# Optimization experiments

Measured on AMD Instinct MI355X. Metric: run time of the kernel, lower is better.

## Reference

```python
import jax, jax.numpy as jnp
import numpy as np

BIN_SZ = 0.02

def setup_inputs() -> dict:
    T, B, D, L, C, H, S = 128, 256, 128, 32, 64, 256, 16
    key = jax.random.key(0)
    ks = iter(jax.random.split(key, 64))
    def nrm(shape, fan_in):
        return jax.random.normal(next(ks), shape, dtype=jnp.float32) / np.float32(np.sqrt(fan_in))
    return dict(
        xs_pre=jax.random.randint(next(ks), (B, T, D), 0, 5).astype(jnp.float32),
        eps0=jax.random.normal(next(ks), (S, B, L), dtype=jnp.float32),
        dW=jax.random.normal(next(ks), (T - 1, S, B, L), dtype=jnp.float32),
        gru_Wih=nrm((3 * H, D), D), gru_Whh=nrm((3 * H, H), H),
        gru_bih=jnp.zeros(3 * H), gru_bhh=jnp.zeros(3 * H),
        enc_W=nrm((C, H), H), enc_b=jnp.zeros(C),
        qz0_W=nrm((2 * L, C), C), qz0_b=jnp.zeros(2 * L),
        fW1=nrm((H, L + C), L + C), fb1=jnp.zeros(H),
        fW2=nrm((H, H), H), fb2=jnp.zeros(H),
        fW3=nrm((L, H), H), fb3=jnp.zeros(L),
        hW1=nrm((H, L), L), hb1=jnp.zeros(H),
        hW2=nrm((H, H), H), hb2=jnp.zeros(H),
        hW3=nrm((L, H), H), hb3=jnp.zeros(L),
        gW1=nrm((L, H), 1), gb1=jnp.zeros((L, H)),
        gW2=nrm((L, H), H), gb2=jnp.zeros(L),
        pz0_mean=jnp.zeros((1, L)), pz0_logstd=jnp.zeros((1, L)),
        C_out=nrm((L, D), L), d_out=jnp.zeros(D),
    )

def _forward(xs_pre, eps0, dW, gru_Wih, gru_Whh, gru_bih, gru_bhh, enc_W, enc_b,
             qz0_W, qz0_b, fW1, fb1, fW2, fb2, fW3, fb3, hW1, hb1, hW2, hb2, hW3, hb3,
             gW1, gb1, gW2, gb2, pz0_mean, pz0_logstd, C_out, d_out):
    xs = jnp.transpose(xs_pre, (1, 0, 2))  # (T,B,D) time-major
    T, B, D = xs.shape
    # --- Encoder: GRU over time-reversed data, linear head, flip back ---
    def gru_step(h, x):
        gi = x @ gru_Wih.T + gru_bih
        gh = h @ gru_Whh.T + gru_bhh
        i_r, i_z, i_n = jnp.split(gi, 3, axis=-1)
        h_r, h_z, h_n = jnp.split(gh, 3, axis=-1)
        r = jax.nn.sigmoid(i_r + h_r)
        u = jax.nn.sigmoid(i_z + h_z)
        n = jnp.tanh(i_n + r * h_n)
        hn = (1.0 - u) * n + u * h
        return hn, hn
    h0 = jnp.zeros((B, gru_Whh.shape[1]), xs.dtype)
    _, hs = jax.lax.scan(gru_step, h0, xs[::-1])
    ctx = (hs @ enc_W.T + enc_b)[::-1]  # (T,B,C)
    # --- initial latent z0 ~ q(z0) ---
    q = ctx[0] @ qz0_W.T + qz0_b
    qz0_mean, qz0_logstd = jnp.split(q, 2, axis=-1)
    z0 = qz0_mean + jnp.exp(qz0_logstd) * eps0  # (S,B,L)
    sp = jax.nn.softplus
    def f_net(i): return sp(sp(i @ fW1.T + fb1) @ fW2.T + fb2) @ fW3.T + fb3
    def h_net(y): return sp(sp(y @ hW1.T + hb1) @ hW2.T + hb2) @ hW3.T + hb3
    def g_fn(y):
        hg = sp(y[..., None] * gW1 + gb1)  # (...,L,H): all diagonal g_nets batched
        return jax.nn.sigmoid(jnp.einsum('...lh,lh->...l', hg, gW2) + gb2) + 0.01
    dt = BIN_SZ
    sq_dt = jnp.sqrt(jnp.asarray(dt, z0.dtype))
    # torchsde euler + searchsorted(right=True): step k uses ctx[min(k+1, T-1)]
    ctx_steps = ctx[jnp.minimum(jnp.arange(T - 1) + 1, T - 1)]  # (T-1,B,C)
    S = z0.shape[0]
    def euler_step(z, inp):
        ctx_i, dw = inp
        ctx_b = jnp.broadcast_to(ctx_i[None], (S,) + ctx_i.shape)
        fv = f_net(jnp.concatenate([z, ctx_b], axis=-1))
        hv = h_net(z)
        gv = g_fn(z)
        u = (fv - hv) / gv
        dlog = 0.5 * jnp.sum(u * u, axis=-1) * dt  # (S,B) logqp increment
        zn = z + fv * dt + gv * (sq_dt * dw)
        return zn, (zn, dlog)
    _, (z_tail, log_ratio) = jax.lax.scan(euler_step, z0, (ctx_steps, dW))
    zs = jnp.concatenate([z0[None], z_tail], axis=0)  # (T,S,B,L)
    zs = jnp.transpose(zs, (1, 0, 2, 3))              # (S,T,B,L)
    log_ratio = jnp.transpose(log_ratio, (1, 0, 2))   # (S,T-1,B)
    # --- Poisson likelihood, rate = bin_sz * exp(linear readout) ---
    log_rate = zs @ C_out + d_out + jnp.log(jnp.asarray(dt, zs.dtype))  # (S,T,B,D)
    ell = xs * log_rate - jnp.exp(log_rate) - jax.lax.lgamma(xs + 1.0)
    log_pxs = ell.sum(-1).sum(1).mean()
    # --- KL(q(z0) || p(z0)) for diagonal Gaussians ---
    kl0 = (pz0_logstd - qz0_logstd
           + (jnp.exp(2.0 * qz0_logstd) + (qz0_mean - pz0_mean) ** 2) / (2.0 * jnp.exp(2.0 * pz0_logstd))
           - 0.5)
    logqp0 = kl0.sum(-1).mean()
    logqp_path = log_ratio.sum(1).mean()
    loss = -log_pxs + logqp0 + logqp_path
    zs_t = jnp.transpose(zs, (0, 2, 1, 3))  # (S,B,T,L)
    m = zs_t.mean(0)
    P_diag = jnp.var(zs_t, axis=0, ddof=1)  # torch.var is unbiased
    return loss, zs_t, m, P_diag

def reference(xs_pre, eps0, dW, gru_Wih, gru_Whh, gru_bih, gru_bhh, enc_W, enc_b,
              qz0_W, qz0_b, fW1, fb1, fW2, fb2, fW3, fb3, hW1, hb1, hW2, hb2, hW3, hb3,
              gW1, gb1, gW2, gb2, pz0_mean, pz0_logstd, C_out, d_out):
    return _forward(xs_pre, eps0, dW, gru_Wih, gru_Whh, gru_bih, gru_bhh, enc_W, enc_b,
                    qz0_W, qz0_b, fW1, fb1, fW2, fb2, fW3, fb3, hW1, hb1, hW2, hb2, hW3, hb3,
                    gW1, gb1, gW2, gb2, pz0_mean, pz0_logstd, C_out, d_out)
```

## Files before the change

### kernel.cpp

```cpp
#include <hip/hip_runtime.h>
#include <math.h>

#define T_ 128
#define B_ 256
#define D_ 128
#define L_ 32
#define C_ 64
#define H_ 256
#define S_ 16
#define R_ 4096
#define NT_ 127
#define DT 0.02f
#define SQDT 0.14142135623730951f

typedef _Float16 h2 __attribute__((ext_vector_type(2)));
typedef _Float16 f16x8 __attribute__((ext_vector_type(8)));
typedef float f32x4m __attribute__((ext_vector_type(4)));
union UH { unsigned u; h2 h; };
union HS { _Float16 f; unsigned short s; };
union U4F { uint4 u; f16x8 h; };

__device__ __forceinline__ float d2(unsigned a, unsigned b, float c){
  UH ua; ua.u = a; UH ub; ub.u = b;
#if defined(__has_builtin)
#if __has_builtin(__builtin_amdgcn_fdot2)
  return __builtin_amdgcn_fdot2(ua.h, ub.h, c, false);
#else
  return fmaf((float)ua.h.x, (float)ub.h.x, fmaf((float)ua.h.y, (float)ub.h.y, c));
#endif
#else
  return fmaf((float)ua.h.x, (float)ub.h.x, fmaf((float)ua.h.y, (float)ub.h.y, c));
#endif
}
__device__ __forceinline__ unsigned pk2(float x, float y){
  UH u; u.h = (h2){(_Float16)x, (_Float16)y}; return u.u;
}
__device__ __forceinline__ unsigned short h1(float x){
  HS t; t.f = (_Float16)x; return t.s;
}
__device__ __forceinline__ float h2f(unsigned short s){
  HS t; t.s = s; return (float)t.f;
}
__device__ __forceinline__ f32x4m mfma16(f16x8 a, f16x8 b, f32x4m c){
  return __builtin_amdgcn_mfma_f32_16x16x32_f16(a, b, c, 0, 0, 0);
}
__device__ __forceinline__ f16x8 ldfragL(const unsigned short* p){
  U4F t; t.u = *(const uint4*)p; return t.h;
}
__device__ __forceinline__ f16x8 ldfragG(const uint4* p){
  U4F t; t.u = *p; return t.h;
}
__device__ __forceinline__ f16x8 ldfragR(uint4 v){
  U4F t; t.u = v; return t.h;
}

__device__ __forceinline__ float sp_(float x){
  return fmaxf(x, 0.f) + __logf(1.f + __expf(-fabsf(x)));
}
__device__ __forceinline__ float sig_(float x){
  return 1.f / (1.f + __expf(-x));
}
__device__ __forceinline__ void dacc4(unsigned av, uint4 w, float a[4]){
  a[0]=d2(av,w.x,a[0]); a[1]=d2(av,w.y,a[1]); a[2]=d2(av,w.z,a[2]); a[3]=d2(av,w.w,a[3]);
}

__device__ __forceinline__ void blk_reduce_add(float v, double* acc){
  for (int o = 32; o > 0; o >>= 1) v += __shfl_down(v, o, 64);
  __shared__ float wpart[4];
  int lane = threadIdx.x & 63, w = threadIdx.x >> 6;
  if (lane == 0) wpart[w] = v;
  __syncthreads();
  if (threadIdx.x == 0) atomicAdd(acc, (double)(wpart[0] + wpart[1] + wpart[2] + wpart[3]));
}

__device__ void do_prep(int i,
                        const float* __restrict__ Wih, const float* __restrict__ Whh,
                        const float* __restrict__ encW,
                        const float* __restrict__ fW1, const float* __restrict__ hW1,
                        const float* __restrict__ fW2, const float* __restrict__ hW2,
                        const float* __restrict__ fW3, const float* __restrict__ hW3,
                        unsigned* WihH, unsigned* WhhH, float* encWT,
                        uint4* fW1B, uint4* hW1B, uint4* fW2B, uint4* hW2B,
                        uint4* fW3B, uint4* hW3B){
  if (i < 49152){ int dp = i / 768, j = i % 768;
    WihH[i] = pk2(Wih[j*128 + 2*dp], Wih[j*128 + 2*dp + 1]); return; }
  i -= 49152;
  if (i < 98304){ int kp = i / 768, j = i % 768;
    WhhH[i] = pk2(Whh[j*256 + 2*kp], Whh[j*256 + 2*kp + 1]); return; }
  i -= 98304;
  if (i < 16384){ int k2 = i >> 6, c = i & 63; encWT[i] = encW[c*256 + k2]; return; }
  i -= 16384;
  if (i < 3072){
    int jt = i / 192, r = i % 192, s = r >> 6, lane = r & 63;
    int col = jt*16 + (lane & 15), kb = s*32 + (lane >> 4)*8;
    const float* src = fW1 + col*96 + kb;
    uint4 v; v.x = pk2(src[0],src[1]); v.y = pk2(src[2],src[3]);
    v.z = pk2(src[4],src[5]); v.w = pk2(src[6],src[7]);
    fW1B[i] = v; return; }
  i -= 3072;
  if (i < 1024){
    int jt = i >> 6, lane = i & 63;
    int col = jt*16 + (lane & 15), kb = (lane >> 4)*8;
    const float* src = hW1 + col*32 + kb;
    uint4 v; v.x = pk2(src[0],src[1]); v.y = pk2(src[2],src[3]);
    v.z = pk2(src[4],src[5]); v.w = pk2(src[6],src[7]);
    hW1B[i] = v; return; }
  i -= 1024;
  if (i < 8192){
    int jt = i >> 9, r = i & 511, s = r >> 6, lane = r & 63;
    int col = jt*16 + (lane & 15), kb = s*32 + (lane >> 4)*8;
    const float* src = fW2 + col*256 + kb;
    uint4 v; v.x = pk2(src[0],src[1]); v.y = pk2(src[2],src[3]);
    v.z = pk2(src[4],src[5]); v.w = pk2(src[6],src[7]);
    fW2B[i] = v; return; }
  i -= 8192;
  if (i < 8192){
    int jt = i >> 9, r = i & 511, s = r >> 6, lane = r & 63;
    int col = jt*16 + (lane & 15), kb = s*32 + (lane >> 4)*8;
    const float* src = hW2 + col*256 + kb;
    uint4 v; v.x = pk2(src[0],src[1]); v.y = pk2(src[2],src[3]);
    v.z = pk2(src[4],src[5]); v.w = pk2(src[6],src[7]);
    hW2B[i] = v; return; }
  i -= 8192;
  if (i < 1024){
    int jt = i >> 9, r = i & 511, s = r >> 6, lane = r & 63;
    int col = jt*16 + (lane & 15), kb = s*32 + (lane >> 4)*8;
    const float* src = fW3 + col*256 + kb;
    uint4 v; v.x = pk2(src[0],src[1]); v.y = pk2(src[2],src[3]);
    v.z = pk2(src[4],src[5]); v.w = pk2(src[6],src[7]);
    fW3B[i] = v; return; }
  i -= 1024;
  if (i < 1024){
    int jt = i >> 9, r = i & 511, s = r >> 6, lane = r & 63;
    int col = jt*16 + (lane & 15), kb = s*32 + (lane >> 4)*8;
    const float* src = hW3 + col*256 + kb;
    uint4 v; v.x = pk2(src[0],src[1]); v.y = pk2(src[2],src[3]);
    v.z = pk2(src[4],src[5]); v.w = pk2(src[6],src[7]);
    hW3B[i] = v; return; }
}

__global__ __launch_bounds__(256) void k_pre(
    const float* __restrict__ Wih, const float* __restrict__ Whh,
    const float* __restrict__ encW,
    const float* __restrict__ fW1, const float* __restrict__ hW1,
    const float* __restrict__ fW2, const float* __restrict__ hW2,
    const float* __restrict__ fW3, const float* __restrict__ hW3,
    const float* __restrict__ gW1, const float* __restrict__ gb1,
    const float* __restrict__ gW2, const float* __restrict__ gb2,
    unsigned* WihH, unsigned* WhhH, float* encWT,
    uint4* fW1B, uint4* hW1B, uint4* fW2B, uint4* hW2B,
    uint4* fW3B, uint4* hW3B, float* gtab, double* accs){
  if (blockIdx.x == 727 && threadIdx.x < 3) accs[threadIdx.x] = 0.0;
  do_prep(blockIdx.x * 256 + threadIdx.x,
          Wih, Whh, encW, fW1, hW1, fW2, hW2, fW3, hW3,
          WihH, WhhH, encWT, fW1B, hW1B, fW2B, hW2B, fW3B, hW3B);
  if (blockIdx.x < 256){
    int l = blockIdx.x >> 3;
    int e = (blockIdx.x & 7) * 256 + threadIdx.x;
    float z = -16.f + (float)e * (1.f / 64.f);
    const float* w1 = gW1 + l * 256;
    const float* b1 = gb1 + l * 256;
    const float* w2 = gW2 + l * 256;
    float s = 0.f;
    #pragma unroll 4
    for (int h = 0; h < 256; ++h)
      s = fmaf(sp_(fmaf(z, w1[h], b1[h])), w2[h], s);
    gtab[l * 2048 + e] = sig_(s + gb2[l]) + 0.01f;
  }
}

__global__ __launch_bounds__(256) void k_gix(
    const float* __restrict__ xs_pre, const unsigned* __restrict__ WihH,
    unsigned short* __restrict__ gixH){
  int kk = blockIdx.x >> 4;
  int b0 = (blockIdx.x & 15) * 16;
  int tid = threadIdx.x;
  int t = 127 - kk;
  __shared__ unsigned x_s[16][64];
  for (int i = tid; i < 16*64; i += 256){
    int r = i >> 6, dp = i & 63;
    const float* xp = xs_pre + ((size_t)(b0 + r)*128 + t)*128 + dp*2;
    x_s[r][dp] = pk2(xp[0], xp[1]);
  }
  __syncthreads();
  float a0[16], a1[16], a2[16];
  #pragma unroll
  for (int r = 0; r < 16; ++r){ a0[r]=0.f; a1[r]=0.f; a2[r]=0.f; }
  for (int dp = 0; dp < 64; ++dp){
    unsigned w0 = WihH[dp*768 + tid];
    unsigned w1 = WihH[dp*768 + 256 + tid];
    unsigned w2 = WihH[dp*768 + 512 + tid];
    #pragma unroll
    for (int r = 0; r < 16; ++r){
      unsigned xv = x_s[r][dp];
      a0[r] = d2(xv, w0, a0[r]);
      a1[r] = d2(xv, w1, a1[r]);
      a2[r] = d2(xv, w2, a2[r]);
    }
  }
  #pragma unroll
  for (int r = 0; r < 16; ++r){
    size_t base = ((size_t)kk*256 + b0 + r)*768;
    gixH[base + tid]       = h1(a0[r]);
    gixH[base + 256 + tid] = h1(a1[r]);
    gixH[base + 512 + tid] = h1(a2[r]);
  }
}

__global__ __launch_bounds__(512, 1) void k_gru_rec(
    const unsigned* __restrict__ WhhH, const float* __restrict__ bih,
    const float* __restrict__ bhh, const unsigned short* __restrict__ gixH,
    float* __restrict__ hsT){
  int tid = threadIdx.x;
  int ks = tid >> 6;
  int lane = tid & 63;
  int j4 = lane * 4;
  int b = blockIdx.x;

  __shared__ float h_s[256];
  __shared__ unsigned h_sH[128];
  __shared__ __align__(16) float part[3][8][256];

  if (tid < 256) h_s[tid] = 0.f;
  if (tid < 128) h_sH[tid] = 0u;

  uint4 w0[16], w1[16], w2[16];
  #pragma unroll
  for (int i = 0; i < 16; ++i){
    const unsigned* wr = WhhH + (ks*16 + i)*768;
    w0[i] = *(const uint4*)(wr + j4);
    w1[i] = *(const uint4*)(wr + 256 + j4);
    w2[i] = *(const uint4*)(wr + 512 + j4);
  }
  __syncthreads();

  for (int k = 0; k < T_; ++k){
    unsigned short pr = 0, pz = 0, pn = 0;
    if (tid < 256){
      size_t gb = ((size_t)k*256 + b)*768;
      pr = gixH[gb + tid];
      pz = gixH[gb + 256 + tid];
      pn = gixH[gb + 512 + tid];
    }
    float a0[4]={0,0,0,0}, a1[4]={0,0,0,0}, a3[4]={0,0,0,0};
    #pragma unroll
    for (int i = 0; i < 16; ++i){
      unsigned hv = h_sH[ks*16 + i];
      dacc4(hv, w0[i], a0);
      dacc4(hv, w1[i], a1);
      dacc4(hv, w2[i], a3);
    }
    *(float4*)&part[0][ks][j4] = make_float4(a0[0],a0[1],a0[2],a0[3]);
    *(float4*)&part[1][ks][j4] = make_float4(a1[0],a1[1],a1[2],a1[3]);
    *(float4*)&part[2][ks][j4] = make_float4(a3[0],a3[1],a3[2],a3[3]);
    __syncthreads();
    if (tid < 256){
      int jj = tid;
      float s0=0.f, s1=0.f, s3=0.f;
      #pragma unroll
      for (int q = 0; q < 8; ++q){
        s0 += part[0][q][jj]; s1 += part[1][q][jj]; s3 += part[2][q][jj];
      }
      float gr = s0 + h2f(pr) + bih[jj] + bhh[jj];
      float gz = s1 + h2f(pz) + bih[256 + jj] + bhh[256 + jj];
      float gnx = h2f(pn) + bih[512 + jj];
      float gnh = s3 + bhh[512 + jj];
      float rr = sig_(gr);
      float uu = sig_(gz);
      float nn = 1.f - 2.f / (1.f + __expf(2.f * (gnx + rr * gnh)));
      float hn = (1.f - uu) * nn + uu * h_s[jj];
      hsT[((size_t)k*256 + b)*256 + jj] = hn;
      h_s[jj] = hn;
      float hnb = __shfl_down(hn, 1, 64);
      if ((tid & 1) == 0) h_sH[jj >> 1] = pk2(hn, hnb);
    }
    __syncthreads();
  }
}

__global__ __launch_bounds__(256) void k_ctx2(
    const float* __restrict__ hsT, const float* __restrict__ encWT,
    const float* __restrict__ encb, float* __restrict__ ctx2){
  int t = blockIdx.x >> 4;
  int b0 = (blockIdx.x & 15) * 16;
  int tid = threadIdx.x;
  __shared__ float h_s[16][256];
  int kk0 = 127 - t;
  for (int i = tid; i < 4096; i += 256){
    int rr = i >> 8, jj = i & 255;
    h_s[rr][jj] = hsT[((size_t)kk0*256 + b0 + rr)*256 + jj];
  }
  __syncthreads();
  float acc0=0, acc1=0, acc2=0, acc3=0;
  int c = tid & 63;
  int bq0 = tid >> 6;
  #pragma unroll 4
  for (int kk = 0; kk < 256; ++kk){
    float wv = encWT[kk*64 + c];
    acc0 = fmaf(h_s[bq0][kk],      wv, acc0);
    acc1 = fmaf(h_s[bq0 + 4][kk],  wv, acc1);
    acc2 = fmaf(h_s[bq0 + 8][kk],  wv, acc2);
    acc3 = fmaf(h_s[bq0 + 12][kk], wv, acc3);
  }
  float bv = encb[c];
  ctx2[(t*256 + b0 + bq0)*64 + c]      = acc0 + bv;
  ctx2[(t*256 + b0 + bq0 + 4)*64 + c]  = acc1 + bv;
  ctx2[(t*256 + b0 + bq0 + 8)*64 + c]  = acc2 + bv;
  ctx2[(t*256 + b0 + bq0 + 12)*64 + c] = acc3 + bv;
}

__global__ __launch_bounds__(256) void k_q0z0(
    const float* __restrict__ ctx2, const float* __restrict__ qW,
    const float* __restrict__ qb, const float* __restrict__ pm,
    const float* __restrict__ pls, const float* __restrict__ eps0,
    float* __restrict__ zs, double* __restrict__ kl_acc){
  int b0 = blockIdx.x * 16;
  int tid = threadIdx.x;
  int lb = tid >> 4;
  int lp = tid & 15;
  int b = b0 + lb;
  __shared__ float qm_s[16][32], qls_s[16][32];
  const float* crow = ctx2 + b * 64;
  float am0 = qb[lp],      as0 = qb[32 + lp];
  float am1 = qb[16 + lp], as1 = qb[48 + lp];
  const float* wm0 = qW + lp * 64;
  const float* ws0 = qW + (32 + lp) * 64;
  const float* wm1 = qW + (16 + lp) * 64;
  const float* ws1 = qW + (48 + lp) * 64;
  for (int c = 0; c < 64; ++c){
    float cv = crow[c];
    am0 = fmaf(cv, wm0[c], am0); as0 = fmaf(cv, ws0[c], as0);
    am1 = fmaf(cv, wm1[c], am1); as1 = fmaf(cv, ws1[c], as1);
  }
  qm_s[lb][lp] = am0;      qls_s[lb][lp] = as0;
  qm_s[lb][16 + lp] = am1; qls_s[lb][16 + lp] = as1;
  float kl = 0.f;
  {
    float plsl = pls[lp], pml = pm[lp];
    float dm = am0 - pml;
    kl += plsl - as0 + (__expf(2.f*as0) + dm*dm) / (2.f*__expf(2.f*plsl)) - 0.5f;
    plsl = pls[16 + lp]; pml = pm[16 + lp];
    dm = am1 - pml;
    kl += plsl - as1 + (__expf(2.f*as1) + dm*dm) / (2.f*__expf(2.f*plsl)) - 0.5f;
  }
  blk_reduce_add(kl, kl_acc);
  int s = tid >> 4, bb = tid & 15;
  int r = s * 256 + b0 + bb;
  #pragma unroll
  for (int l = 0; l < 32; l += 4){
    float4 e = *(const float4*)(eps0 + (size_t)r*32 + l);
    float4 z;
    z.x = fmaf(__expf(qls_s[bb][l    ]), e.x, qm_s[bb][l    ]);
    z.y = fmaf(__expf(qls_s[bb][l + 1]), e.y, qm_s[bb][l + 1]);
    z.z = fmaf(__expf(qls_s[bb][l + 2]), e.z, qm_s[bb][l + 2]);
    z.w = fmaf(__expf(qls_s[bb][l + 3]), e.w, qm_s[bb][l + 3]);
    *(float4*)(zs + (size_t)r * (T_ * L_) + l) = z;
  }
}

__global__ __launch_bounds__(512, 1) void k_sde_all(
    const float* __restrict__ ctx2,
    const uint4* __restrict__ fW1B, const float* __restrict__ fb1,
    const uint4* __restrict__ hW1B, const float* __restrict__ hb1,
    const uint4* __restrict__ fW2B, const float* __restrict__ fb2,
    const uint4* __restrict__ hW2B, const float* __restrict__ hb2,
    const uint4* __restrict__ fW3B, const uint4* __restrict__ hW3B,
    const float* __restrict__ fb3, const float* __restrict__ hb3,
    const float* __restrict__ gtab,
    const float* __restrict__ dW, float* __restrict__ zs,
    double* __restrict__ u2_acc){
  int tid = threadIdx.x;
  int r0 = blockIdx.x * 16;
  int b0 = r0 & 255;
  int w  = tid >> 6;
  int ln = tid & 63;
  int frow = ln & 15;
  int kg = ln >> 4;
  int crow0 = kg * 4;
  int lane32 = tid & 31;
  int row16 = tid >> 5;

  __shared__ __align__(16) unsigned short z_sH[16][32];
  __shared__ __align__(16) unsigned short ctx_sH[16][64];
  __shared__ __align__(16) unsigned short a1H[2][16][256];
  __shared__ __align__(16) unsigned short a2H[2][16][256];
  __shared__ float fh_part[2][2][16][32];

  float zreg = zs[(size_t)(r0 + row16) * 4096 + lane32];
  {
    int idx = row16*32 + (((((lane32) >> 3) ^ (row16 & 3)) << 3) | (lane32 & 7));
    ((unsigned short*)z_sH)[idx] = h1(zreg);
  }
  float u2loc = 0.f;

  uint4 wf2r[16], wh2r[16];
  #pragma unroll
  for (int q = 0; q < 2; ++q){
    #pragma unroll
    for (int s = 0; s < 8; ++s){
      wf2r[q*8 + s] = fW2B[((2*w + q)*8 + s)*64 + ln];
      wh2r[q*8 + s] = hW2B[((2*w + q)*8 + s)*64 + ln];
    }
  }

  const unsigned short* a1b0 = &a1H[0][0][0];
  const unsigned short* a1b1 = &a1H[1][0][0];
  const unsigned short* a2b0 = &a2H[0][0][0];
  const unsigned short* a2b1 = &a2H[1][0][0];

  for (int k = 0; k < NT_; ++k){
    __syncthreads();
    if (tid < 256){
      int rr = tid >> 4, c4 = (tid & 15) * 4;
      float4 v = *(const float4*)(ctx2 + ((size_t)(k + 1)*256 + b0 + rr)*64 + c4);
      uint2 p = make_uint2(pk2(v.x, v.y), pk2(v.z, v.w));
      int idx = rr*64 + ((((c4 >> 3) ^ (rr & 7)) << 3) | (c4 & 7));
      *(uint2*)(((unsigned short*)ctx_sH) + idx) = p;
    }
    __syncthreads();

    float gv;
    {
      float tpos = fminf(fmaxf((zreg + 16.f) * 64.f, 0.f), 2046.99f);
      int i0 = (int)tpos;
      float fr = tpos - (float)i0;
      const float* tl = gtab + lane32 * 2048 + i0;
      float t0 = tl[0], t1 = tl[1];
      gv = fmaf(fr, t1 - t0, t0);
    }

    {
      f16x8 zA  = ldfragL(((const unsigned short*)z_sH) + frow*32 + ((kg ^ (frow & 3)) << 3));
      f16x8 cA0 = ldfragL(((const unsigned short*)ctx_sH) + frow*64 + (((kg       ) ^ (frow & 7)) << 3));
      f16x8 cA1 = ldfragL(((const unsigned short*)ctx_sH) + frow*64 + (((4 + kg   ) ^ (frow & 7)) << 3));
      #pragma unroll
      for (int q = 0; q < 2; ++q){
        int jt = 2*w + q;
        const uint4* bp = fW1B + (jt*3)*64 + ln;
        f32x4m acc = {0.f, 0.f, 0.f, 0.f};
        acc = mfma16(zA,  ldfragG(bp),        acc);
        acc = mfma16(cA0, ldfragG(bp + 64),   acc);
        acc = mfma16(cA1, ldfragG(bp + 128),  acc);
        int col = jt*16 + frow;
        float bv = fb1[col];
        #pragma unroll
        for (int r = 0; r < 4; ++r){
          int row = crow0 + r;
          ((unsigned short*)a1H)[0*4096 + row*256 + ((((col >> 3) ^ (row & 7)) << 3) | (col & 7))]
            = h1(sp_(acc[r] + bv));
        }
      }
      #pragma unroll
      for (int q = 0; q < 2; ++q){
        int jt = 2*w + q;
        f32x4m acc = {0.f, 0.f, 0.f, 0.f};
        acc = mfma16(zA, ldfragG(hW1B + jt*64 + ln), acc);
        int col = jt*16 + frow;
        float bv = hb1[col];
        #pragma unroll
        for (int r = 0; r < 4; ++r){
          int row = crow0 + r;
          ((unsigned short*)a1H)[1*4096 + row*256 + ((((col >> 3) ^ (row & 7)) << 3) | (col & 7))]
            = h1(sp_(acc[r] + bv));
        }
      }
    }
    __syncthreads();

    {
      f16x8 fr8[8];
      #pragma unroll
      for (int s = 0; s < 8; ++s)
        fr8[s] = ldfragL(a1b0 + frow*256 + (((s*4 + kg) ^ (frow & 7)) << 3));
      #pragma unroll
      for (int q = 0; q < 2; ++q){
        int jt = 2*w + q;
        f32x4m acc = {0.f, 0.f, 0.f, 0.f};
        #pragma unroll
        for (int s = 0; s < 8; ++s)
          acc = mfma16(fr8[s], ldfragR(wf2r[q*8 + s]), acc);
        int col = jt*16 + frow;
        float bv = fb2[col];
        #pragma unroll
        for (int r = 0; r < 4; ++r){
          int row = crow0 + r;
          ((unsigned short*)a2H)[0*4096 + row*256 + ((((col >> 3) ^ (row & 7)) << 3) | (col & 7))]
            = h1(sp_(acc[r] + bv));
        }
      }
      #pragma unroll
      for (int s = 0; s < 8; ++s)
        fr8[s] = ldfragL(a1b1 + frow*256 + (((s*4 + kg) ^ (frow & 7)) << 3));
      #pragma unroll
      for (int q = 0; q < 2; ++q){
        int jt = 2*w + q;
        f32x4m acc = {0.f, 0.f, 0.f, 0.f};
        #pragma unroll
        for (int s = 0; s < 8; ++s)
          acc = mfma16(fr8[s], ldfragR(wh2r[q*8 + s]), acc);
        int col = jt*16 + frow;
        float bv = hb2[col];
        #pragma unroll
        for (int r = 0; r < 4; ++r){
          int row = crow0 + r;
          ((unsigned short*)a2H)[1*4096 + row*256 + ((((col >> 3) ^ (row & 7)) << 3) | (col & 7))]
            = h1(sp_(acc[r] + bv));
        }
      }
    }
    __syncthreads();

    {
      int kh  = w >> 2;
      int net = (w >> 1) & 1;
      int jt  = w & 1;
      const unsigned short* ab = net ? a2b1 : a2b0;
      const uint4* bb = (net ? hW3B : fW3B) + (jt*8 + kh*4)*64 + ln;
      f32x4m acc = {0.f, 0.f, 0.f, 0.f};
      #pragma unroll
      for (int q = 0; q < 4; ++q){
        int s = kh*4 + q;
        f16x8 af = ldfragL(ab + frow*256 + (((s*4 + kg) ^ (frow & 7)) << 3));
        acc = mfma16(af, ldfragG(bb + q*64), acc);
      }
      int col = jt*16 + frow;
      #pragma unroll
      for (int r = 0; r < 4; ++r)
        fh_part[kh][net][crow0 + r][col] = acc[r];
    }
    __syncthreads();

    {
      float fv = fh_part[0][0][row16][lane32] + fh_part[1][0][row16][lane32] + fb3[lane32];
      float hv = fh_part[0][1][row16][lane32] + fh_part[1][1][row16][lane32] + hb3[lane32];
      float uu = (fv - hv) / gv;
      u2loc = fmaf(uu, uu, u2loc);
      int rr = r0 + row16;
      float dwv = dW[((size_t)k*4096 + rr)*32 + lane32];
      float zn = zreg + fv*DT + gv*(SQDT*dwv);
      zreg = zn;
      zs[((size_t)rr*128 + (k + 1))*32 + lane32] = zn;
      int idx = row16*32 + ((((lane32 >> 3) ^ (row16 & 3)) << 3) | (lane32 & 7));
      ((unsigned short*)z_sH)[idx] = h1(zn);
    }
  }

  for (int o = 32; o > 0; o >>= 1) u2loc += __shfl_down(u2loc, o, 64);
  __shared__ float wp[8];
  if ((tid & 63) == 0) wp[tid >> 6] = u2loc;
  __syncthreads();
  if (tid == 0){
    float s = 0.f;
    #pragma unroll
    for (int q = 0; q < 8; ++q) s += wp[q];
    atomicAdd(u2_acc, (double)s);
  }
}

__global__ __launch_bounds__(256) void k_poismv(
    const float* __restrict__ zs, const float* __restrict__ Cw,
    const float* __restrict__ db, const float* __restrict__ xs_pre,
    double* __restrict__ ell_acc, float* __restrict__ m, float* __restrict__ P){
  if (blockIdx.x < 4096){
    const int N = S_ * B_ * T_ * D_;
    const int stride = 4096 * 256;
    float local = 0.f;
    for (int i = blockIdx.x * 256 + threadIdx.x; i < N; i += stride){
      int d = i & 127; int row = i >> 7;
      int t = row & 127; int b = (row >> 7) & 255;
      const float* zrow = zs + (size_t)row * L_;
      float lr = db[d] - 3.912023005428146f;
      #pragma unroll 8
      for (int l = 0; l < L_; ++l) lr = fmaf(zrow[l], Cw[l * D_ + d], lr);
      float xv = xs_pre[(b * T_ + t) * D_ + d];
      int xi = (int)(xv + 0.5f);
      float lg = (xi <= 1) ? 0.f : (xi == 2 ? 0.6931471805599453f :
                 (xi == 3 ? 1.791759469228055f : 3.1780538303479458f));
      local += xv * lr - __expf(lr) - lg;
    }
    blk_reduce_add(local, ell_acc);
  } else {
    int i = (blockIdx.x - 4096) * 256 + threadIdx.x;
    float x[S_];
    float s = 0.f;
    #pragma unroll
    for (int q = 0; q < S_; ++q){ x[q] = zs[(size_t)q * (B_ * T_ * L_) + i]; s += x[q]; }
    float mu = s * (1.f / S_);
    float v = 0.f;
    #pragma unroll
    for (int q = 0; q < S_; ++q){ float dd = x[q] - mu; v = fmaf(dd, dd, v); }
    m[i] = mu;
    P[i] = v * (1.f / (S_ - 1));
  }
}

__global__ void k_fin(const double* __restrict__ accs, float* __restrict__ out){
  double log_pxs = accs[0] / 4096.0;
  double logqp0 = accs[1] / 256.0;
  double logqp_path = 0.5 * 0.02 * accs[2] / 4096.0;
  out[0] = (float)(-log_pxs + logqp0 + logqp_path);
}

extern "C" void kernel_launch(void* const* d_in, const int* in_sizes, int n_in,
                              void* d_out, int out_size, void* d_ws, size_t ws_size,
                              hipStream_t stream) {
  const float* xs_pre = (const float*)d_in[0];
  const float* eps0   = (const float*)d_in[1];
  const float* dW     = (const float*)d_in[2];
  const float* Wih    = (const float*)d_in[3];
  const float* Whh    = (const float*)d_in[4];
  const float* bih    = (const float*)d_in[5];
  const float* bhh    = (const float*)d_in[6];
  const float* encW   = (const float*)d_in[7];
  const float* encb   = (const float*)d_in[8];
  const float* qW     = (const float*)d_in[9];
  const float* qb     = (const float*)d_in[10];
  const float* fW1    = (const float*)d_in[11];
  const float* fb1    = (const float*)d_in[12];
  const float* fW2    = (const float*)d_in[13];
  const float* fb2    = (const float*)d_in[14];
  const float* fW3    = (const float*)d_in[15];
  const float* fb3    = (const float*)d_in[16];
  const float* hW1    = (const float*)d_in[17];
  const float* hb1    = (const float*)d_in[18];
  const float* hW2    = (const float*)d_in[19];
  const float* hb2    = (const float*)d_in[20];
  const float* hW3    = (const float*)d_in[21];
  const float* hb3    = (const float*)d_in[22];
  const float* gW1    = (const float*)d_in[23];
  const float* gb1    = (const float*)d_in[24];
  const float* gW2    = (const float*)d_in[25];
  const float* gb2    = (const float*)d_in[26];
  const float* pm     = (const float*)d_in[27];
  const float* pls    = (const float*)d_in[28];
  const float* Cw     = (const float*)d_in[29];
  const float* db     = (const float*)d_in[30];

  float* out = (float*)d_out;
  float* zs  = out + 1;
  float* m   = out + 1 + 16777216;
  float* P   = m + 1048576;

  unsigned short* gixH = (unsigned short*)zs;

  double* accs = (double*)d_ws;
  float* wf = (float*)d_ws + 16;
  float* hsT   = wf; wf += T_ * B_ * H_;
  float* ctx2  = wf; wf += T_ * B_ * C_;
  unsigned* WihH = (unsigned*)wf; wf += 49152;
  unsigned* WhhH = (unsigned*)wf; wf += 98304;
  float* encWT = wf; wf += 16384;
  uint4* fW1B = (uint4*)wf; wf += 12288;
  uint4* hW1B = (uint4*)wf; wf += 4096;
  uint4* fW2B = (uint4*)wf; wf += 32768;
  uint4* hW2B = (uint4*)wf; wf += 32768;
  uint4* fW3B = (uint4*)wf; wf += 4096;
  uint4* hW3B = (uint4*)wf; wf += 4096;
  float* gtab  = wf; wf += 65536;
  size_t need = (size_t)(wf - (float*)d_ws) * 4;
  if (ws_size < need) return;

  k_pre<<<728, 256, 0, stream>>>(Wih, Whh, encW, fW1, hW1, fW2, hW2, fW3, hW3,
                                 gW1, gb1, gW2, gb2,
                                 WihH, WhhH, encWT, fW1B, hW1B, fW2B, hW2B,
                                 fW3B, hW3B, gtab, accs);
  k_gix<<<2048, 256, 0, stream>>>(xs_pre, WihH, gixH);
  k_gru_rec<<<256, 512, 0, stream>>>(WhhH, bih, bhh, gixH, hsT);
  k_ctx2<<<2048, 256, 0, stream>>>(hsT, encWT, encb, ctx2);
  k_q0z0<<<16, 256, 0, stream>>>(ctx2, qW, qb, pm, pls, eps0, zs, accs + 1);
  k_sde_all<<<256, 512, 0, stream>>>(ctx2,
                                     fW1B, fb1, hW1B, hb1,
                                     fW2B, fb2, hW2B, hb2,
                                     fW3B, hW3B, fb3, hb3,
                                     gtab, dW, zs, accs + 2);
  k_poismv<<<8192, 256, 0, stream>>>(zs, Cw, db, xs_pre, accs + 0, m, P);
  k_fin<<<1, 1, 0, stream>>>(accs, out);
}
```

Before: 1.279 ms.

## Fuse GRU input projection into recurrence and merge small tail kernels

The GRU input-projection kernel is folded into the recurrent kernel: each block now computes its own batch row's input gates from an LDS-staged copy of the time-reversed inputs before running the recurrence. The q(z0)/z0 sampling work moves into the t==0 blocks of the context projection kernel, and the final loss reduction moves into the Poisson/moments kernel through an atomic ticket held in a fourth accumulator slot. This removes three kernel launches and the ctx2 re-read for z0. In exchange, the input projection runs on only 256 single-occupancy blocks with an uneven split, since only half the threads handle the third gate, instead of 2048 well-occupied blocks. The gate results also still round-trip through global memory.

Result: slower. 2.035 ms (+59.1%).

```diff
diff --git a/kernel.cpp b/kernel.cpp
--- a/kernel.cpp
+++ b/kernel.cpp
@@ -150,7 +150,7 @@
     unsigned* WihH, unsigned* WhhH, float* encWT,
     uint4* fW1B, uint4* hW1B, uint4* fW2B, uint4* hW2B,
     uint4* fW3B, uint4* hW3B, float* gtab, double* accs){
-  if (blockIdx.x == 727 && threadIdx.x < 3) accs[threadIdx.x] = 0.0;
+  if (blockIdx.x == 727 && threadIdx.x < 4) accs[threadIdx.x] = 0.0;
   do_prep(blockIdx.x * 256 + threadIdx.x,
           Wih, Whh, encW, fW1, hW1, fW2, hW2, fW3, hW3,
           WihH, WhhH, encWT, fW1B, hW1B, fW2B, hW2B, fW3B, hW3B);
@@ -169,61 +169,66 @@
   }
 }
 
-__global__ __launch_bounds__(256) void k_gix(
+__global__ __launch_bounds__(512, 1) void k_gru_all2(
     const float* __restrict__ xs_pre, const unsigned* __restrict__ WihH,
-    unsigned short* __restrict__ gixH){
-  int kk = blockIdx.x >> 4;
-  int b0 = (blockIdx.x & 15) * 16;
-  int tid = threadIdx.x;
-  int t = 127 - kk;
-  __shared__ unsigned x_s[16][64];
-  for (int i = tid; i < 16*64; i += 256){
-    int r = i >> 6, dp = i & 63;
-    const float* xp = xs_pre + ((size_t)(b0 + r)*128 + t)*128 + dp*2;
-    x_s[r][dp] = pk2(xp[0], xp[1]);
-  }
-  __syncthreads();
-  float a0[16], a1[16], a2[16];
-  #pragma unroll
-  for (int r = 0; r < 16; ++r){ a0[r]=0.f; a1[r]=0.f; a2[r]=0.f; }
-  for (int dp = 0; dp < 64; ++dp){
-    unsigned w0 = WihH[dp*768 + tid];
-    unsigned w1 = WihH[dp*768 + 256 + tid];
-    unsigned w2 = WihH[dp*768 + 512 + tid];
-    #pragma unroll
-    for (int r = 0; r < 16; ++r){
-      unsigned xv = x_s[r][dp];
-      a0[r] = d2(xv, w0, a0[r]);
-      a1[r] = d2(xv, w1, a1[r]);
-      a2[r] = d2(xv, w2, a2[r]);
-    }
-  }
-  #pragma unroll
-  for (int r = 0; r < 16; ++r){
-    size_t base = ((size_t)kk*256 + b0 + r)*768;
-    gixH[base + tid]       = h1(a0[r]);
-    gixH[base + 256 + tid] = h1(a1[r]);
-    gixH[base + 512 + tid] = h1(a2[r]);
-  }
-}
-
-__global__ __launch_bounds__(512, 1) void k_gru_rec(
     const unsigned* __restrict__ WhhH, const float* __restrict__ bih,
-    const float* __restrict__ bhh, const unsigned short* __restrict__ gixH,
+    const float* __restrict__ bhh, unsigned short* __restrict__ gixH,
     float* __restrict__ hsT){
   int tid = threadIdx.x;
+  int b = blockIdx.x;
+
+  __shared__ unsigned x_all[128][64];
+  __shared__ float h_s[256];
+  __shared__ unsigned h_sH[128];
+  __shared__ __align__(16) float part[3][8][256];
+
+  for (int i = tid; i < 8192; i += 512){
+    int t = i >> 6, dp = i & 63;
+    const float* xp = xs_pre + ((size_t)b*128 + t)*128 + dp*2;
+    x_all[127 - t][dp] = pk2(xp[0], xp[1]);
+  }
+  if (tid < 256) h_s[tid] = 0.f;
+  if (tid < 128) h_sH[tid] = 0u;
+  __syncthreads();
+
+  {
+    int j = tid;
+    for (int kc = 0; kc < 128; kc += 16){
+      float acc[16];
+      #pragma unroll
+      for (int q = 0; q < 16; ++q) acc[q] = 0.f;
+      for (int dp = 0; dp < 64; ++dp){
+        unsigned w = WihH[dp*768 + j];
+        #pragma unroll
+        for (int q = 0; q < 16; ++q)
+          acc[q] = d2(x_all[kc + q][dp], w, acc[q]);
+      }
+      #pragma unroll
+      for (int q = 0; q < 16; ++q)
+        gixH[((size_t)(kc + q)*256 + b)*768 + j] = h1(acc[q]);
+    }
+  }
+  if (tid < 256){
+    int j = 512 + tid;
+    for (int kc = 0; kc < 128; kc += 16){
+      float acc[16];
+      #pragma unroll
+      for (int q = 0; q < 16; ++q) acc[q] = 0.f;
+      for (int dp = 0; dp < 64; ++dp){
+        unsigned w = WihH[dp*768 + j];
+        #pragma unroll
+        for (int q = 0; q < 16; ++q)
+          acc[q] = d2(x_all[kc + q][dp], w, acc[q]);
+      }
+      #pragma unroll
+      for (int q = 0; q < 16; ++q)
+        gixH[((size_t)(kc + q)*256 + b)*768 + j] = h1(acc[q]);
+    }
+  }
+
   int ks = tid >> 6;
   int lane = tid & 63;
   int j4 = lane * 4;
-  int b = blockIdx.x;
-
-  __shared__ float h_s[256];
-  __shared__ unsigned h_sH[128];
-  __shared__ __align__(16) float part[3][8][256];
-
-  if (tid < 256) h_s[tid] = 0.f;
-  if (tid < 128) h_sH[tid] = 0u;
-
   uint4 w0[16], w1[16], w2[16];
   #pragma unroll
   for (int i = 0; i < 16; ++i){
@@ -278,9 +283,13 @@
   }
 }
 
-__global__ __launch_bounds__(256) void k_ctx2(
+__global__ __launch_bounds__(256) void k_ctx2q(
     const float* __restrict__ hsT, const float* __restrict__ encWT,
-    const float* __restrict__ encb, float* __restrict__ ctx2){
+    const float* __restrict__ encb, float* __restrict__ ctx2,
+    const float* __restrict__ qW, const float* __restrict__ qb,
+    const float* __restrict__ pm, const float* __restrict__ pls,
+    const float* __restrict__ eps0, float* __restrict__ zs,
+    double* __restrict__ kl_acc){
   int t = blockIdx.x >> 4;
   int b0 = (blockIdx.x & 15) * 16;
   int tid = threadIdx.x;
@@ -303,58 +312,58 @@
     acc3 = fmaf(h_s[bq0 + 12][kk], wv, acc3);
   }
   float bv = encb[c];
-  ctx2[(t*256 + b0 + bq0)*64 + c]      = acc0 + bv;
-  ctx2[(t*256 + b0 + bq0 + 4)*64 + c]  = acc1 + bv;
-  ctx2[(t*256 + b0 + bq0 + 8)*64 + c]  = acc2 + bv;
-  ctx2[(t*256 + b0 + bq0 + 12)*64 + c] = acc3 + bv;
-}
-
-__global__ __launch_bounds__(256) void k_q0z0(
-    const float* __restrict__ ctx2, const float* __restrict__ qW,
-    const float* __restrict__ qb, const float* __restrict__ pm,
-    const float* __restrict__ pls, const float* __restrict__ eps0,
-    float* __restrict__ zs, double* __restrict__ kl_acc){
-  int b0 = blockIdx.x * 16;
-  int tid = threadIdx.x;
-  int lb = tid >> 4;
-  int lp = tid & 15;
-  int b = b0 + lb;
-  __shared__ float qm_s[16][32], qls_s[16][32];
-  const float* crow = ctx2 + b * 64;
-  float am0 = qb[lp],      as0 = qb[32 + lp];
-  float am1 = qb[16 + lp], as1 = qb[48 + lp];
-  const float* wm0 = qW + lp * 64;
-  const float* ws0 = qW + (32 + lp) * 64;
-  const float* wm1 = qW + (16 + lp) * 64;
-  const float* ws1 = qW + (48 + lp) * 64;
-  for (int c = 0; c < 64; ++c){
-    float cv = crow[c];
-    am0 = fmaf(cv, wm0[c], am0); as0 = fmaf(cv, ws0[c], as0);
-    am1 = fmaf(cv, wm1[c], am1); as1 = fmaf(cv, ws1[c], as1);
-  }
-  qm_s[lb][lp] = am0;      qls_s[lb][lp] = as0;
-  qm_s[lb][16 + lp] = am1; qls_s[lb][16 + lp] = as1;
-  float kl = 0.f;
-  {
-    float plsl = pls[lp], pml = pm[lp];
-    float dm = am0 - pml;
-    kl += plsl - as0 + (__expf(2.f*as0) + dm*dm) / (2.f*__expf(2.f*plsl)) - 0.5f;
-    plsl = pls[16 + lp]; pml = pm[16 + lp];
-    dm = am1 - pml;
-    kl += plsl - as1 + (__expf(2.f*as1) + dm*dm) / (2.f*__expf(2.f*plsl)) - 0.5f;
-  }
-  blk_reduce_add(kl, kl_acc);
-  int s = tid >> 4, bb = tid & 15;
-  int r = s * 256 + b0 + bb;
-  #pragma unroll
-  for (int l = 0; l < 32; l += 4){
-    float4 e = *(const float4*)(eps0 + (size_t)r*32 + l);
-    float4 z;
-    z.x = fmaf(__expf(qls_s[bb][l    ]), e.x, qm_s[bb][l    ]);
-    z.y = fmaf(__expf(qls_s[bb][l + 1]), e.y, qm_s[bb][l + 1]);
-    z.z = fmaf(__expf(qls_s[bb][l + 2]), e.z, qm_s[bb][l + 2]);
-    z.w = fmaf(__expf(qls_s[bb][l + 3]), e.w, qm_s[bb][l + 3]);
-    *(float4*)(zs + (size_t)r * (T_ * L_) + l) = z;
+  acc0 += bv; acc1 += bv; acc2 += bv; acc3 += bv;
+  ctx2[(t*256 + b0 + bq0)*64 + c]      = acc0;
+  ctx2[(t*256 + b0 + bq0 + 4)*64 + c]  = acc1;
+  ctx2[(t*256 + b0 + bq0 + 8)*64 + c]  = acc2;
+  ctx2[(t*256 + b0 + bq0 + 12)*64 + c] = acc3;
+
+  if (t == 0){
+    __shared__ float ctx_l[16][64];
+    __shared__ float qm_s[16][32], qls_s[16][32];
+    ctx_l[bq0][c]      = acc0;
+    ctx_l[bq0 + 4][c]  = acc1;
+    ctx_l[bq0 + 8][c]  = acc2;
+    ctx_l[bq0 + 12][c] = acc3;
+    __syncthreads();
+    int lb = tid >> 4;
+    int lp = tid & 15;
+    const float* crow = ctx_l[lb];
+    float am0 = qb[lp],      as0 = qb[32 + lp];
+    float am1 = qb[16 + lp], as1 = qb[48 + lp];
+    const float* wm0 = qW + lp * 64;
+    const float* ws0 = qW + (32 + lp) * 64;
+    const float* wm1 = qW + (16 + lp) * 64;
+    const float* ws1 = qW + (48 + lp) * 64;
+    for (int cc = 0; cc < 64; ++cc){
+      float cv = crow[cc];
+      am0 = fmaf(cv, wm0[cc], am0); as0 = fmaf(cv, ws0[cc], as0);
+      am1 = fmaf(cv, wm1[cc], am1); as1 = fmaf(cv, ws1[cc], as1);
+    }
+    qm_s[lb][lp] = am0;      qls_s[lb][lp] = as0;
+    qm_s[lb][16 + lp] = am1; qls_s[lb][16 + lp] = as1;
+    float kl = 0.f;
+    {
+      float plsl = pls[lp], pml = pm[lp];
+      float dm = am0 - pml;
+      kl += plsl - as0 + (__expf(2.f*as0) + dm*dm) / (2.f*__expf(2.f*plsl)) - 0.5f;
+      plsl = pls[16 + lp]; pml = pm[16 + lp];
+      dm = am1 - pml;
+      kl += plsl - as1 + (__expf(2.f*as1) + dm*dm) / (2.f*__expf(2.f*plsl)) - 0.5f;
+    }
+    blk_reduce_add(kl, kl_acc);
+    int s = tid >> 4, bb = tid & 15;
+    int r = s * 256 + b0 + bb;
+    #pragma unroll
+    for (int l = 0; l < 32; l += 4){
+      float4 e = *(const float4*)(eps0 + (size_t)r*32 + l);
+      float4 z;
+      z.x = fmaf(__expf(qls_s[bb][l    ]), e.x, qm_s[bb][l    ]);
+      z.y = fmaf(__expf(qls_s[bb][l + 1]), e.y, qm_s[bb][l + 1]);
+      z.z = fmaf(__expf(qls_s[bb][l + 2]), e.z, qm_s[bb][l + 2]);
+      z.w = fmaf(__expf(qls_s[bb][l + 3]), e.w, qm_s[bb][l + 3]);
+      *(float4*)(zs + (size_t)r * (T_ * L_) + l) = z;
+    }
   }
 }
 
@@ -560,7 +569,8 @@
 __global__ __launch_bounds__(256) void k_poismv(
     const float* __restrict__ zs, const float* __restrict__ Cw,
     const float* __restrict__ db, const float* __restrict__ xs_pre,
-    double* __restrict__ ell_acc, float* __restrict__ m, float* __restrict__ P){
+    double* __restrict__ accs, float* __restrict__ m, float* __restrict__ P,
+    float* __restrict__ out){
   if (blockIdx.x < 4096){
     const int N = S_ * B_ * T_ * D_;
     const int stride = 4096 * 256;
@@ -578,7 +588,7 @@
                  (xi == 3 ? 1.791759469228055f : 3.1780538303479458f));
       local += xv * lr - __expf(lr) - lg;
     }
-    blk_reduce_add(local, ell_acc);
+    blk_reduce_add(local, accs + 0);
   } else {
     int i = (blockIdx.x - 4096) * 256 + threadIdx.x;
     float x[S_];
@@ -592,13 +602,17 @@
     m[i] = mu;
     P[i] = v * (1.f / (S_ - 1));
   }
-}
-
-__global__ void k_fin(const double* __restrict__ accs, float* __restrict__ out){
-  double log_pxs = accs[0] / 4096.0;
-  double logqp0 = accs[1] / 256.0;
-  double logqp_path = 0.5 * 0.02 * accs[2] / 4096.0;
-  out[0] = (float)(-log_pxs + logqp0 + logqp_path);
+  __threadfence();
+  if (threadIdx.x == 0){
+    unsigned* ticket = (unsigned*)(accs + 3);
+    unsigned tk = atomicAdd(ticket, 1u);
+    if (tk == 8191u){
+      double log_pxs = accs[0] / 4096.0;
+      double logqp0 = accs[1] / 256.0;
+      double logqp_path = 0.5 * 0.02 * accs[2] / 4096.0;
+      out[0] = (float)(-log_pxs + logqp0 + logqp_path);
+    }
+  }
 }
 
 extern "C" void kernel_launch(void* const* d_in, const int* in_sizes, int n_in,
@@ -664,15 +678,13 @@
                                  gW1, gb1, gW2, gb2,
                                  WihH, WhhH, encWT, fW1B, hW1B, fW2B, hW2B,
                                  fW3B, hW3B, gtab, accs);
-  k_gix<<<2048, 256, 0, stream>>>(xs_pre, WihH, gixH);
-  k_gru_rec<<<256, 512, 0, stream>>>(WhhH, bih, bhh, gixH, hsT);
-  k_ctx2<<<2048, 256, 0, stream>>>(hsT, encWT, encb, ctx2);
-  k_q0z0<<<16, 256, 0, stream>>>(ctx2, qW, qb, pm, pls, eps0, zs, accs + 1);
+  k_gru_all2<<<256, 512, 0, stream>>>(xs_pre, WihH, WhhH, bih, bhh, gixH, hsT);
+  k_ctx2q<<<2048, 256, 0, stream>>>(hsT, encWT, encb, ctx2, qW, qb, pm, pls,
+                                    eps0, zs, accs + 1);
   k_sde_all<<<256, 512, 0, stream>>>(ctx2,
                                      fW1B, fb1, hW1B, hb1,
                                      fW2B, fb2, hW2B, hb2,
                                      fW3B, hW3B, fb3, hb3,
                                      gtab, dW, zs, accs + 2);
-  k_poismv<<<8192, 256, 0, stream>>>(zs, Cw, db, xs_pre, accs + 0, m, P);
-  k_fin<<<1, 1, 0, stream>>>(accs, out);
-}
+  k_poismv<<<8192, 256, 0, stream>>>(zs, Cw, db, xs_pre, accs, m, P, out);
+}
```
